# Optimization experiments

Measured on AMD Instinct MI355X. Metric: run time of the kernel, lower is better.

Reference implementation:

```python
import jax, jax.numpy as jnp
import numpy as np

EPS = 1e-5
N_NODES = 50000


def batchnorm(x, gamma, beta):
    # training-mode BatchNorm1d: batch mean, biased variance
    mean = jnp.mean(x, axis=0)
    var = jnp.mean(jnp.square(x - mean), axis=0)
    return (x - mean) * jax.lax.rsqrt(var + EPS) * gamma + beta


def setup_inputs() -> dict:
    key = jax.random.key(0)
    ks = jax.random.split(key, 8)
    N, E, D_IN, D_H, D_OUT = N_NODES, 800000, 128, 128, 128
    feat = jax.random.normal(ks[0], (N, D_IN), dtype=jnp.float32)
    w = jax.random.uniform(ks[1], (E,), dtype=jnp.float32)
    # xavier_uniform with relu gain for Q and W
    gain = float(np.sqrt(2.0))
    bq = gain * np.sqrt(6.0 / (D_IN + D_H))
    bw = gain * np.sqrt(6.0 / (D_IN + D_H + D_OUT))
    Q_w = jax.random.uniform(ks[2], (D_H, D_IN), minval=-bq, maxval=bq, dtype=jnp.float32)
    W_w = jax.random.uniform(ks[3], (D_OUT, D_IN + D_H), minval=-bw, maxval=bw, dtype=jnp.float32)
    Q_b = jnp.zeros((D_H,), jnp.float32)
    W_b = jnp.zeros((D_OUT,), jnp.float32)
    gamma2 = jnp.ones((D_OUT,), jnp.float32)
    beta2 = jnp.zeros((D_OUT,), jnp.float32)
    src = jax.random.randint(ks[4], (E,), 0, N, dtype=jnp.int32)
    dst = jax.random.randint(ks[5], (E,), 0, N, dtype=jnp.int32)
    return {"feat": feat, "w": w, "Q_w": Q_w, "Q_b": Q_b, "W_w": W_w,
            "W_b": W_b, "gamma2": gamma2, "beta2": beta2, "src": src, "dst": dst}


def reference(feat, w, Q_w, Q_b, W_w, W_b, gamma2, beta2, src, dst):
    N = feat.shape[0]
    # h = dropout(bnorm_two(relu(Q(feat))))  (dropout=0 -> identity; source reuses bnorm_two)
    h = batchnorm(jax.nn.relu(feat @ Q_w.T + Q_b), gamma2, beta2)  # [N, H]
    # weighted neighbor mean: sum_e w_e * h[src_e] scattered to dst, / sum_e w_e
    num = jax.ops.segment_sum(w[:, None] * h[src], dst, num_segments=N)  # [N, H]
    den = jax.ops.segment_sum(w, dst, num_segments=N)  # [N]
    has_msg = den[:, None] != 0
    agg = jnp.where(has_msg, num / jnp.where(has_msg, den[:, None], 1.0), h)
    rst = jnp.concatenate([feat, agg], axis=1) @ W_w.T + W_b  # [N, OUT]
    rst = batchnorm(jax.nn.relu(rst), gamma2, beta2)
    denom = jnp.linalg.norm(rst, axis=1, keepdims=True)
    return rst / jnp.where(denom == 0, 1.0, denom)
```

## Files before the change

kernel.cpp:

```cpp
#include <hip/hip_runtime.h>
#include <stdint.h>


#define BN_EPS 1e-5f
#define NSLOT 32

typedef __attribute__((ext_vector_type(8))) short bf16x8;
typedef __attribute__((ext_vector_type(4))) float f32x4;

static __device__ __forceinline__ unsigned short f2bf(float f) {
    uint32_t u = __builtin_bit_cast(uint32_t, f);
    u += 0x7fffu + ((u >> 16) & 1u);
    return (unsigned short)(u >> 16);
}
static __device__ __forceinline__ float bf_lo(uint32_t u) {
    return __builtin_bit_cast(float, u << 16);
}
static __device__ __forceinline__ float bf_hi(uint32_t u) {
    return __builtin_bit_cast(float, u & 0xffff0000u);
}

static __device__ __forceinline__ void cast_blk(
    const float* __restrict__ src, unsigned short* __restrict__ dst,
    int n, int blk)
{
    int i = (blk * 256 + threadIdx.x) * 4;
    if (i + 3 < n) {
        float4 v = *(const float4*)(src + i);
        ushort4 o;
        o.x = f2bf(v.x); o.y = f2bf(v.y); o.z = f2bf(v.z); o.w = f2bf(v.w);
        *(ushort4*)(dst + i) = o;
    } else {
        for (int j = i; j < n; ++j) dst[j] = f2bf(src[j]);
    }
}

__global__ __launch_bounds__(256) void k_pre(
    const float* __restrict__ feat, unsigned short* __restrict__ featb, int nf,
    const int* __restrict__ dst, int* __restrict__ ccnt, int E, int CB, int HB,
    const float* __restrict__ Qw, unsigned short* __restrict__ Qwb,
    const float* __restrict__ Ww, unsigned short* __restrict__ Wwb)
{
    int b = (int)blockIdx.x;
    if (b < CB) { cast_blk(feat, featb, nf, b); return; }
    b -= CB;
    if (b >= HB) {
        b -= HB;
        if (b < 16) cast_blk(Qw, Qwb, 128 * 128, b);
        else        cast_blk(Ww, Wwb, 128 * 256, b - 16);
        return;
    }
    __shared__ int hcnt[128];
    const int tid = threadIdx.x;
    if (tid < 128) hcnt[tid] = 0;
    __syncthreads();
    const int base_e = b * 2048;
#pragma unroll
    for (int j = 0; j < 8; ++j) {
        int e = base_e + j * 256 + tid;
        if (e < E) atomicAdd(&hcnt[dst[e] >> 9], 1);
    }
    __syncthreads();
    if (tid < 128 && hcnt[tid] > 0) atomicAdd(&ccnt[tid], hcnt[tid]);
}

__global__ __launch_bounds__(128) void k_coffs(
    const int* __restrict__ ccnt, int* __restrict__ coffs,
    int* __restrict__ gcur, int* __restrict__ offs, int N, int E)
{
    __shared__ int w0sum;
    const int t = threadIdx.x;
    const int lane = t & 63, wv = t >> 6;
    int v = ccnt[t];
    int incl = v;
#pragma unroll
    for (int o = 1; o < 64; o <<= 1) {
        int u = __shfl_up(incl, o, 64);
        if (lane >= o) incl += u;
    }
    if (wv == 0 && lane == 63) w0sum = incl;
    __syncthreads();
    int excl = incl - v + (wv ? w0sum : 0);
    coffs[t] = excl;
    gcur[t]  = excl;
    if (t == 127) { coffs[128] = excl + v; offs[N] = E; }
}

template<int K>
static __device__ __forceinline__ void gemm_body(
    int bid,
    const unsigned short* __restrict__ A_lo,
    const unsigned short* __restrict__ A_hi,
    const unsigned short* __restrict__ Bb,
    const float* __restrict__ bias,
    float* __restrict__ Y,
    double* __restrict__ sum, double* __restrict__ sumsq, int N)
{
    constexpr int SA = 72;
    __shared__ unsigned short As[64 * SA];
    __shared__ unsigned short Bs[128 * SA];
    __shared__ float bsum_s[128], bsq_s[128];

    const int tid  = threadIdx.x;
    const int lane = tid & 63;
    const int wv   = tid >> 6;
    const int wr   = wv >> 1;
    const int wc   = wv & 1;
    const int m15  = lane & 15;
    const int quad = lane >> 4;
    const int r0   = bid * 64;

    if (tid < 128) { bsum_s[tid] = 0.f; bsq_s[tid] = 0.f; }

    f32x4 acc[2][4];
#pragma unroll
    for (int rt = 0; rt < 2; ++rt)
#pragma unroll
        for (int ct = 0; ct < 4; ++ct)
            acc[rt][ct] = (f32x4){0.f, 0.f, 0.f, 0.f};

    for (int kc = 0; kc < K; kc += 64) {
        const unsigned short* Ap = (kc < 128) ? A_lo : A_hi;
        const int koff = kc & 127;
#pragma unroll
        for (int i = 0; i < 2; ++i) {
            int idx = i * 256 + tid;
            int row = idx >> 3, seg = idx & 7;
            int gr  = r0 + row; if (gr >= N) gr = N - 1;
            uint4 v = *(const uint4*)(Ap + (size_t)gr * 128 + koff + seg * 8);
            *(uint4*)(As + row * SA + seg * 8) = v;
        }
#pragma unroll
        for (int i = 0; i < 4; ++i) {
            int idx = i * 256 + tid;
            int row = idx >> 3, seg = idx & 7;
            uint4 v = *(const uint4*)(Bb + (size_t)row * K + kc + seg * 8);
            *(uint4*)(Bs + row * SA + seg * 8) = v;
        }
        __syncthreads();

#pragma unroll
        for (int ks = 0; ks < 64; ks += 32) {
            bf16x8 af[2], bfr[4];
#pragma unroll
            for (int rt = 0; rt < 2; ++rt)
                af[rt] = *(const bf16x8*)(As + (wr * 32 + rt * 16 + m15) * SA + ks + quad * 8);
#pragma unroll
            for (int ct = 0; ct < 4; ++ct)
                bfr[ct] = *(const bf16x8*)(Bs + (wc * 64 + ct * 16 + m15) * SA + ks + quad * 8);
#pragma unroll
            for (int rt = 0; rt < 2; ++rt)
#pragma unroll
                for (int ct = 0; ct < 4; ++ct)
                    acc[rt][ct] = __builtin_amdgcn_mfma_f32_16x16x32_bf16(
                        af[rt], bfr[ct], acc[rt][ct], 0, 0, 0);
        }
        __syncthreads();
    }

#pragma unroll
    for (int ct = 0; ct < 4; ++ct) {
        int col = wc * 64 + ct * 16 + m15;
        float bz = bias[col];
        float s = 0.f, q = 0.f;
#pragma unroll
        for (int rt = 0; rt < 2; ++rt) {
#pragma unroll
            for (int reg = 0; reg < 4; ++reg) {
                int row = r0 + wr * 32 + rt * 16 + quad * 4 + reg;
                float vv = fmaxf(acc[rt][ct][reg] + bz, 0.f);
                if (row < N) {
                    Y[(size_t)row * 128 + col] = vv;
                } else {
                    vv = 0.f;
                }
                s += vv; q = fmaf(vv, vv, q);
            }
        }
        s += __shfl_xor(s, 16, 64); s += __shfl_xor(s, 32, 64);
        q += __shfl_xor(q, 16, 64); q += __shfl_xor(q, 32, 64);
        if (quad == 0) {
            atomicAdd(&bsum_s[col], s);
            atomicAdd(&bsq_s[col], q);
        }
    }
    __syncthreads();
    if (tid < 128) {
        const int slot = (bid & (NSLOT - 1)) * 128;
        atomicAdd(&sum[slot + tid],   (double)bsum_s[tid]);
        atomicAdd(&sumsq[slot + tid], (double)bsq_s[tid]);
    }
}

__global__ __launch_bounds__(128) void bn_coef(
    const double* __restrict__ sum, const double* __restrict__ sumsq,
    const float* __restrict__ gamma, const float* __restrict__ beta,
    float* __restrict__ a, float* __restrict__ b, double invN)
{
    const int t = threadIdx.x;
    double ms = 0.0, qs = 0.0;
#pragma unroll
    for (int s = 0; s < NSLOT; ++s) {
        ms += sum[s * 128 + t];
        qs += sumsq[s * 128 + t];
    }
    float mean = (float)(ms * invN);
    float var  = (float)(qs * invN) - mean * mean;
    float sc = rsqrtf(var + BN_EPS) * gamma[t];
    a[t] = sc;
    b[t] = fmaf(-mean, sc, beta[t]);
}

static __device__ __forceinline__ void bin_body(
    int bid,
    const int* __restrict__ src, const int* __restrict__ dst,
    const float* __restrict__ w, int* __restrict__ gcur,
    int4* __restrict__ tmp, int E)
{
    __shared__ int hcnt[128];
    __shared__ int hbase[128];
    const int tid = threadIdx.x;
    if (tid < 128) hcnt[tid] = 0;
    __syncthreads();

    int d8[8], s8[8], slot8[8];
    float w8[8];
#pragma unroll
    for (int j = 0; j < 8; ++j) {
        int e = bid * 2048 + j * 256 + tid;
        if (e < E) {
            d8[j] = dst[e]; s8[j] = src[e]; w8[j] = w[e];
            slot8[j] = atomicAdd(&hcnt[d8[j] >> 9], 1);
        } else d8[j] = -1;
    }
    __syncthreads();
    if (tid < 128 && hcnt[tid] > 0)
        hbase[tid] = atomicAdd(&gcur[tid], hcnt[tid]);
    __syncthreads();
#pragma unroll
    for (int j = 0; j < 8; ++j) {
        if (d8[j] >= 0) {
            int pos = hbase[d8[j] >> 9] + slot8[j];
            tmp[pos] = make_int4(s8[j], __float_as_int(w8[j]), d8[j], 0);
        }
    }
}

__global__ __launch_bounds__(256) void k_bin_gemm(
    const int* __restrict__ src, const int* __restrict__ dst,
    const float* __restrict__ w, int* __restrict__ gcur,
    int4* __restrict__ tmp, int E, int HB,
    const unsigned short* __restrict__ featb,
    const unsigned short* __restrict__ Qwb, const float* __restrict__ Qb,
    float* __restrict__ y1,
    double* __restrict__ sum, double* __restrict__ sumsq, int N)
{
    if ((int)blockIdx.x < HB)
        bin_body(blockIdx.x, src, dst, w, gcur, tmp, E);
    else
        gemm_body<128>(blockIdx.x - HB, featb, featb, Qwb, Qb, y1, sum, sumsq, N);
}

static __device__ __forceinline__ void refine_body(
    int b,
    const int4* __restrict__ tmp, const int* __restrict__ coffs,
    int* __restrict__ offs, int2* __restrict__ epack, int N)
{
    __shared__ int hist[512];
    __shared__ int wpre[4];
    const int d0   = b << 9;
    const int dlim = min(512, N - d0);
    const int tid  = threadIdx.x;
    const int lane = tid & 63, wv = tid >> 6;
    const int start = coffs[b];
    const int end   = coffs[b + 1];

    hist[tid] = 0; hist[tid + 256] = 0;
    __syncthreads();

    for (int p = start + tid; p < end; p += 256)
        atomicAdd(&hist[tmp[p].z - d0], 1);
    __syncthreads();

    int v0 = hist[2 * tid], v1 = hist[2 * tid + 1];
    int s = v0 + v1;
    int incl = s;
#pragma unroll
    for (int o = 1; o < 64; o <<= 1) {
        int t = __shfl_up(incl, o, 64);
        if (lane >= o) incl += t;
    }
    if (lane == 63) wpre[wv] = incl;
    __syncthreads();
    if (tid == 0) {
        int r = 0;
#pragma unroll
        for (int i = 0; i < 4; ++i) { int t = wpre[i]; wpre[i] = r; r += t; }
    }
    __syncthreads();
    int e0 = start + wpre[wv] + incl - s;
    if (2 * tid < dlim)     offs[d0 + 2 * tid]     = e0;
    if (2 * tid + 1 < dlim) offs[d0 + 2 * tid + 1] = e0 + v0;
    hist[2 * tid]     = e0;
    hist[2 * tid + 1] = e0 + v0;
    __syncthreads();

    for (int p = start + tid; p < end; p += 256) {
        int4 rec = tmp[p];
        int pos = atomicAdd(&hist[rec.z - d0], 1);
        epack[pos] = make_int2(rec.x, rec.y);
    }
}

__global__ __launch_bounds__(256) void k_refine_apply(
    const int4* __restrict__ tmp, const int* __restrict__ coffs,
    int* __restrict__ offs, int2* __restrict__ epack, int N, int NB,
    const float* __restrict__ y,
    const float* __restrict__ a, const float* __restrict__ b,
    unsigned short* __restrict__ h, int n)
{
    if ((int)blockIdx.x < NB) {
        refine_body(blockIdx.x, tmp, coffs, offs, epack, N);
    } else {
        int i = ((blockIdx.x - NB) * 256 + threadIdx.x) * 4;
        if (i >= n) return;
        int c = i & 127;
        float4 v  = *(const float4*)(y + i);
        float4 av = *(const float4*)(a + c);
        float4 bv = *(const float4*)(b + c);
        ushort4 o;
        o.x = f2bf(fmaf(av.x, v.x, bv.x));
        o.y = f2bf(fmaf(av.y, v.y, bv.y));
        o.z = f2bf(fmaf(av.z, v.z, bv.z));
        o.w = f2bf(fmaf(av.w, v.w, bv.w));
        *(ushort4*)(h + i) = o;
    }
}

__global__ __launch_bounds__(256) void gather_agg(
    const unsigned short* __restrict__ h,
    const int* __restrict__ offs, const int2* __restrict__ epack,
    unsigned short* __restrict__ aggb, int N)
{
    const int r    = (int)((blockIdx.x * 256u + threadIdx.x) >> 6);
    const int lane = threadIdx.x & 63;
    if (r >= N) return;
    int p = offs[r];
    const int end = offs[r + 1];
    float nx = 0.f, ny = 0.f, den = 0.f;
    for (; p + 3 < end; p += 4) {
        int2 e0 = epack[p],     e1 = epack[p + 1];
        int2 e2 = epack[p + 2], e3 = epack[p + 3];
        uint32_t u0 = *(const uint32_t*)(h + (size_t)e0.x * 128 + 2 * lane);
        uint32_t u1 = *(const uint32_t*)(h + (size_t)e1.x * 128 + 2 * lane);
        uint32_t u2 = *(const uint32_t*)(h + (size_t)e2.x * 128 + 2 * lane);
        uint32_t u3 = *(const uint32_t*)(h + (size_t)e3.x * 128 + 2 * lane);
        float w0 = __int_as_float(e0.y), w1 = __int_as_float(e1.y);
        float w2 = __int_as_float(e2.y), w3 = __int_as_float(e3.y);
        nx = fmaf(w0, bf_lo(u0), nx); ny = fmaf(w0, bf_hi(u0), ny);
        nx = fmaf(w1, bf_lo(u1), nx); ny = fmaf(w1, bf_hi(u1), ny);
        nx = fmaf(w2, bf_lo(u2), nx); ny = fmaf(w2, bf_hi(u2), ny);
        nx = fmaf(w3, bf_lo(u3), nx); ny = fmaf(w3, bf_hi(u3), ny);
        den += (w0 + w1) + (w2 + w3);
    }
    for (; p < end; ++p) {
        int2 e0 = epack[p];
        float w0 = __int_as_float(e0.y);
        uint32_t u0 = *(const uint32_t*)(h + (size_t)e0.x * 128 + 2 * lane);
        nx = fmaf(w0, bf_lo(u0), nx); ny = fmaf(w0, bf_hi(u0), ny);
        den += w0;
    }
    float2 outv;
    if (den != 0.f) {
        float inv = 1.f / den;
        outv.x = nx * inv; outv.y = ny * inv;
    } else {
        uint32_t u = *(const uint32_t*)(h + (size_t)r * 128 + 2 * lane);
        outv.x = bf_lo(u); outv.y = bf_hi(u);
    }
    ushort2 ao; ao.x = f2bf(outv.x); ao.y = f2bf(outv.y);
    *(ushort2*)&aggb[(size_t)r * 128 + 2 * lane] = ao;
}

__global__ __launch_bounds__(256) void gemm_bn2(
    const unsigned short* __restrict__ A_lo,
    const unsigned short* __restrict__ A_hi,
    const unsigned short* __restrict__ Bb,
    const float* __restrict__ bias,
    float* __restrict__ Y,
    double* __restrict__ sum, double* __restrict__ sumsq, int N)
{
    gemm_body<256>(blockIdx.x, A_lo, A_hi, Bb, bias, Y, sum, sumsq, N);
}

__global__ __launch_bounds__(256) void finalize(
    const float* __restrict__ Y2,
    const float* __restrict__ a, const float* __restrict__ b,
    float* __restrict__ out, int N)
{
    __shared__ float sa[128], sb[128];
    const int t = threadIdx.x;
    if (t < 128) { sa[t] = a[t]; sb[t] = b[t]; }
    __syncthreads();
    const int row  = (int)((blockIdx.x * 256u + t) >> 6);
    const int lane = t & 63;
    if (row >= N) return;
    const size_t base = (size_t)row * 128;
    float v0 = fmaf(sa[lane],      Y2[base + lane],      sb[lane]);
    float v1 = fmaf(sa[lane + 64], Y2[base + lane + 64], sb[lane + 64]);
    float ss = fmaf(v0, v0, v1 * v1);
#pragma unroll
    for (int o = 32; o; o >>= 1) ss += __shfl_xor(ss, o, 64);
    float nrm = sqrtf(ss);
    float inv = (nrm == 0.f) ? 1.f : 1.f / nrm;
    out[base + lane]      = v0 * inv;
    out[base + lane + 64] = v1 * inv;
}

extern "C" void kernel_launch(void* const* d_in, const int* in_sizes, int n_in,
                              void* d_out, int out_size, void* d_ws, size_t ws_size,
                              hipStream_t stream)
{
    const float* feat   = (const float*)d_in[0];
    const float* w      = (const float*)d_in[1];
    const float* Q_w    = (const float*)d_in[2];
    const float* Q_b    = (const float*)d_in[3];
    const float* W_w    = (const float*)d_in[4];
    const float* W_b    = (const float*)d_in[5];
    const float* gamma2 = (const float*)d_in[6];
    const float* beta2  = (const float*)d_in[7];
    const int*   src    = (const int*)d_in[8];
    const int*   dst    = (const int*)d_in[9];

    const int N = in_sizes[0] / 128;
    const int E = in_sizes[1];

    float*          y1    = (float*)d_ws;
    unsigned short* featb = (unsigned short*)(y1 + (size_t)N * 128);
    unsigned short* aggb  = featb + (size_t)N * 128;
    unsigned short* h_bf  = aggb + (size_t)N * 128;
    int4*  tmp    = (int4*)(h_bf + (size_t)N * 128);
    int2*  epack  = (int2*)(tmp + E);
    int*   offs   = (int*)(epack + E);
    int*   coffs  = offs + (N + 1);
    int*   gcur   = coffs + 129;
    float* coefs  = (float*)(gcur + 128);
    float* a1 = coefs, *b1 = coefs + 128, *a2 = coefs + 256, *b2 = coefs + 384;
    uintptr_t qp = ((uintptr_t)(coefs + 512) + 15) & ~(uintptr_t)15;
    unsigned short* Qwb = (unsigned short*)qp;
    unsigned short* Wwb = Qwb + 128 * 128;
    uintptr_t sp = ((uintptr_t)(Wwb + 128 * 256) + 15) & ~(uintptr_t)15;
    double* stats = (double*)sp;
    double* sum1   = stats;
    double* sumsq1 = stats + NSLOT * 128;
    double* sum2   = stats + 2 * NSLOT * 128;
    double* sumsq2 = stats + 3 * NSLOT * 128;
    int*   ccnt   = (int*)(stats + 4 * NSLOT * 128);

    hipMemsetAsync(stats, 0,
                   4 * NSLOT * 128 * sizeof(double) + 128 * sizeof(int),
                   stream);

    const double invN = 1.0 / (double)N;
    const int GB = (N + 63) / 64;
    const int NB = (N + 511) >> 9;
    const int CB = (N * 128 / 4 + 255) / 256;
    const int HB = (E + 2047) / 2048;
    const int AB = (N * 128 / 4 + 255) / 256;
    const int QB = 16;
    const int WB = 32;

    k_pre<<<CB + HB + QB + WB, 256, 0, stream>>>(
        feat, featb, N * 128, dst, ccnt, E, CB, HB,
        Q_w, Qwb, W_w, Wwb);
    k_coffs<<<1, 128, 0, stream>>>(ccnt, coffs, gcur, offs, N, E);

    k_bin_gemm<<<HB + GB, 256, 0, stream>>>(
        src, dst, w, gcur, tmp, E, HB,
        featb, Qwb, Q_b, y1, sum1, sumsq1, N);
    bn_coef<<<1, 128, 0, stream>>>(sum1, sumsq1, gamma2, beta2, a1, b1, invN);

    k_refine_apply<<<NB + AB, 256, 0, stream>>>(
        tmp, coffs, offs, epack, N, NB,
        y1, a1, b1, h_bf, N * 128);

    gather_agg<<<(N * 64 + 255) / 256, 256, 0, stream>>>(h_bf, offs, epack, aggb, N);

    gemm_bn2<<<GB, 256, 0, stream>>>(
        featb, aggb, Wwb, W_b, y1 , sum2, sumsq2, N);
    bn_coef<<<1, 128, 0, stream>>>(sum2, sumsq2, gamma2, beta2, a2, b2, invN);
    finalize<<<(N * 64 + 255) / 256, 256, 0, stream>>>(
        y1, a2, b2, (float*)d_out, N);
}
```

Before: 234.4 us.

## Fold first BatchNorm apply into neighbor gather and store pre-BN activations as bf16

The first GEMM now writes relu output directly as bf16 instead of fp32, and the separate elementwise BN-apply pass that produced h is removed. Because BN is affine and the weights are normalized by their sum, the gather aggregates raw activations and applies the BN scale and shift afterwards. The bn_coef launch is merged into the refine kernel as an extra block. The gather is also restructured so each half-wave handles alternate edges with 8-byte loads, reduced by a cross-half shuffle. This cuts one full-size read and write pass plus a launch, at the cost of bf16 rounding before normalization rather than after.

Measured after the change: 227.7 us. 1.03x faster.

```diff
diff --git a/kernel.cpp b/kernel.cpp
--- a/kernel.cpp
+++ b/kernel.cpp
@@ -86,14 +86,14 @@
     if (t == 127) { coffs[128] = excl + v; offs[N] = E; }
 }
 
-template<int K>
+template<int K, bool OUT_BF16>
 static __device__ __forceinline__ void gemm_body(
     int bid,
     const unsigned short* __restrict__ A_lo,
     const unsigned short* __restrict__ A_hi,
     const unsigned short* __restrict__ Bb,
     const float* __restrict__ bias,
-    float* __restrict__ Y,
+    void* __restrict__ Yv,
     double* __restrict__ sum, double* __restrict__ sumsq, int N)
 {
     constexpr int SA = 72;
@@ -170,7 +170,10 @@
                 int row = r0 + wr * 32 + rt * 16 + quad * 4 + reg;
                 float vv = fmaxf(acc[rt][ct][reg] + bz, 0.f);
                 if (row < N) {
-                    Y[(size_t)row * 128 + col] = vv;
+                    if constexpr (OUT_BF16)
+                        ((unsigned short*)Yv)[(size_t)row * 128 + col] = f2bf(vv);
+                    else
+                        ((float*)Yv)[(size_t)row * 128 + col] = vv;
                 } else {
                     vv = 0.f;
                 }
@@ -192,12 +195,11 @@
     }
 }
 
-__global__ __launch_bounds__(128) void bn_coef(
-    const double* __restrict__ sum, const double* __restrict__ sumsq,
+static __device__ __forceinline__ void bn_coef_body(
+    int t, const double* __restrict__ sum, const double* __restrict__ sumsq,
     const float* __restrict__ gamma, const float* __restrict__ beta,
     float* __restrict__ a, float* __restrict__ b, double invN)
 {
-    const int t = threadIdx.x;
     double ms = 0.0, qs = 0.0;
 #pragma unroll
     for (int s = 0; s < NSLOT; ++s) {
@@ -209,6 +211,14 @@
     float sc = rsqrtf(var + BN_EPS) * gamma[t];
     a[t] = sc;
     b[t] = fmaf(-mean, sc, beta[t]);
+}
+
+__global__ __launch_bounds__(128) void bn_coef(
+    const double* __restrict__ sum, const double* __restrict__ sumsq,
+    const float* __restrict__ gamma, const float* __restrict__ beta,
+    float* __restrict__ a, float* __restrict__ b, double invN)
+{
+    bn_coef_body(threadIdx.x, sum, sumsq, gamma, beta, a, b, invN);
 }
 
 static __device__ __forceinline__ void bin_body(
@@ -252,13 +262,14 @@
     int4* __restrict__ tmp, int E, int HB,
     const unsigned short* __restrict__ featb,
     const unsigned short* __restrict__ Qwb, const float* __restrict__ Qb,
-    float* __restrict__ y1,
+    unsigned short* __restrict__ y1b,
     double* __restrict__ sum, double* __restrict__ sumsq, int N)
 {
     if ((int)blockIdx.x < HB)
         bin_body(blockIdx.x, src, dst, w, gcur, tmp, E);
     else
-        gemm_body<128>(blockIdx.x - HB, featb, featb, Qwb, Qb, y1, sum, sumsq, N);
+        gemm_body<128, true>(blockIdx.x - HB, featb, featb, Qwb, Qb, y1b,
+                             sum, sumsq, N);
 }
 
 static __device__ __forceinline__ void refine_body(
@@ -312,74 +323,86 @@
     }
 }
 
-__global__ __launch_bounds__(256) void k_refine_apply(
+__global__ __launch_bounds__(256) void k_bnref(
+    const double* __restrict__ sum, const double* __restrict__ sumsq,
+    const float* __restrict__ gamma, const float* __restrict__ beta,
+    float* __restrict__ a, float* __restrict__ b, double invN,
     const int4* __restrict__ tmp, const int* __restrict__ coffs,
-    int* __restrict__ offs, int2* __restrict__ epack, int N, int NB,
-    const float* __restrict__ y,
+    int* __restrict__ offs, int2* __restrict__ epack, int N)
+{
+    if (blockIdx.x == 0) {
+        if (threadIdx.x < 128)
+            bn_coef_body(threadIdx.x, sum, sumsq, gamma, beta, a, b, invN);
+        return;
+    }
+    refine_body((int)blockIdx.x - 1, tmp, coffs, offs, epack, N);
+}
+
+__global__ __launch_bounds__(256) void gather_agg(
+    const unsigned short* __restrict__ y1b,
+    const int* __restrict__ offs, const int2* __restrict__ epack,
     const float* __restrict__ a, const float* __restrict__ b,
-    unsigned short* __restrict__ h, int n)
-{
-    if ((int)blockIdx.x < NB) {
-        refine_body(blockIdx.x, tmp, coffs, offs, epack, N);
-    } else {
-        int i = ((blockIdx.x - NB) * 256 + threadIdx.x) * 4;
-        if (i >= n) return;
-        int c = i & 127;
-        float4 v  = *(const float4*)(y + i);
-        float4 av = *(const float4*)(a + c);
-        float4 bv = *(const float4*)(b + c);
-        ushort4 o;
-        o.x = f2bf(fmaf(av.x, v.x, bv.x));
-        o.y = f2bf(fmaf(av.y, v.y, bv.y));
-        o.z = f2bf(fmaf(av.z, v.z, bv.z));
-        o.w = f2bf(fmaf(av.w, v.w, bv.w));
-        *(ushort4*)(h + i) = o;
-    }
-}
-
-__global__ __launch_bounds__(256) void gather_agg(
-    const unsigned short* __restrict__ h,
-    const int* __restrict__ offs, const int2* __restrict__ epack,
     unsigned short* __restrict__ aggb, int N)
 {
     const int r    = (int)((blockIdx.x * 256u + threadIdx.x) >> 6);
     const int lane = threadIdx.x & 63;
+    const int li   = lane & 31;
+    const int hf   = lane >> 5;
     if (r >= N) return;
     int p = offs[r];
     const int end = offs[r + 1];
-    float nx = 0.f, ny = 0.f, den = 0.f;
+    float ac0 = 0.f, ac1 = 0.f, ac2 = 0.f, ac3 = 0.f, den = 0.f;
     for (; p + 3 < end; p += 4) {
-        int2 e0 = epack[p],     e1 = epack[p + 1];
-        int2 e2 = epack[p + 2], e3 = epack[p + 3];
-        uint32_t u0 = *(const uint32_t*)(h + (size_t)e0.x * 128 + 2 * lane);
-        uint32_t u1 = *(const uint32_t*)(h + (size_t)e1.x * 128 + 2 * lane);
-        uint32_t u2 = *(const uint32_t*)(h + (size_t)e2.x * 128 + 2 * lane);
-        uint32_t u3 = *(const uint32_t*)(h + (size_t)e3.x * 128 + 2 * lane);
-        float w0 = __int_as_float(e0.y), w1 = __int_as_float(e1.y);
-        float w2 = __int_as_float(e2.y), w3 = __int_as_float(e3.y);
-        nx = fmaf(w0, bf_lo(u0), nx); ny = fmaf(w0, bf_hi(u0), ny);
-        nx = fmaf(w1, bf_lo(u1), nx); ny = fmaf(w1, bf_hi(u1), ny);
-        nx = fmaf(w2, bf_lo(u2), nx); ny = fmaf(w2, bf_hi(u2), ny);
-        nx = fmaf(w3, bf_lo(u3), nx); ny = fmaf(w3, bf_hi(u3), ny);
-        den += (w0 + w1) + (w2 + w3);
-    }
-    for (; p < end; ++p) {
-        int2 e0 = epack[p];
-        float w0 = __int_as_float(e0.y);
-        uint32_t u0 = *(const uint32_t*)(h + (size_t)e0.x * 128 + 2 * lane);
-        nx = fmaf(w0, bf_lo(u0), nx); ny = fmaf(w0, bf_hi(u0), ny);
-        den += w0;
-    }
-    float2 outv;
+        int2 ea = epack[p + hf];
+        int2 eb = epack[p + 2 + hf];
+        uint2 ua = *(const uint2*)(y1b + (size_t)ea.x * 128 + 4 * li);
+        uint2 ub = *(const uint2*)(y1b + (size_t)eb.x * 128 + 4 * li);
+        float wa = __int_as_float(ea.y), wb = __int_as_float(eb.y);
+        ac0 = fmaf(wa, bf_lo(ua.x), ac0); ac1 = fmaf(wa, bf_hi(ua.x), ac1);
+        ac2 = fmaf(wa, bf_lo(ua.y), ac2); ac3 = fmaf(wa, bf_hi(ua.y), ac3);
+        ac0 = fmaf(wb, bf_lo(ub.x), ac0); ac1 = fmaf(wb, bf_hi(ub.x), ac1);
+        ac2 = fmaf(wb, bf_lo(ub.y), ac2); ac3 = fmaf(wb, bf_hi(ub.y), ac3);
+        den += wa + wb;
+    }
+    for (; p + 1 < end; p += 2) {
+        int2 ea = epack[p + hf];
+        uint2 ua = *(const uint2*)(y1b + (size_t)ea.x * 128 + 4 * li);
+        float wa = __int_as_float(ea.y);
+        ac0 = fmaf(wa, bf_lo(ua.x), ac0); ac1 = fmaf(wa, bf_hi(ua.x), ac1);
+        ac2 = fmaf(wa, bf_lo(ua.y), ac2); ac3 = fmaf(wa, bf_hi(ua.y), ac3);
+        den += wa;
+    }
+    if (p < end && hf == 0) {
+        int2 ea = epack[p];
+        uint2 ua = *(const uint2*)(y1b + (size_t)ea.x * 128 + 4 * li);
+        float wa = __int_as_float(ea.y);
+        ac0 = fmaf(wa, bf_lo(ua.x), ac0); ac1 = fmaf(wa, bf_hi(ua.x), ac1);
+        ac2 = fmaf(wa, bf_lo(ua.y), ac2); ac3 = fmaf(wa, bf_hi(ua.y), ac3);
+        den += wa;
+    }
+    ac0 += __shfl_xor(ac0, 32, 64);
+    ac1 += __shfl_xor(ac1, 32, 64);
+    ac2 += __shfl_xor(ac2, 32, 64);
+    ac3 += __shfl_xor(ac3, 32, 64);
+    den += __shfl_xor(den, 32, 64);
+    if (hf) return;
+    const int c = 4 * li;
+    float4 av = *(const float4*)(a + c);
+    float4 bv = *(const float4*)(b + c);
+    float m0, m1, m2, m3;
     if (den != 0.f) {
         float inv = 1.f / den;
-        outv.x = nx * inv; outv.y = ny * inv;
+        m0 = ac0 * inv; m1 = ac1 * inv; m2 = ac2 * inv; m3 = ac3 * inv;
     } else {
-        uint32_t u = *(const uint32_t*)(h + (size_t)r * 128 + 2 * lane);
-        outv.x = bf_lo(u); outv.y = bf_hi(u);
-    }
-    ushort2 ao; ao.x = f2bf(outv.x); ao.y = f2bf(outv.y);
-    *(ushort2*)&aggb[(size_t)r * 128 + 2 * lane] = ao;
+        uint2 u = *(const uint2*)(y1b + (size_t)r * 128 + c);
+        m0 = bf_lo(u.x); m1 = bf_hi(u.x); m2 = bf_lo(u.y); m3 = bf_hi(u.y);
+    }
+    ushort4 o;
+    o.x = f2bf(fmaf(av.x, m0, bv.x));
+    o.y = f2bf(fmaf(av.y, m1, bv.y));
+    o.z = f2bf(fmaf(av.z, m2, bv.z));
+    o.w = f2bf(fmaf(av.w, m3, bv.w));
+    *(ushort4*)(aggb + (size_t)r * 128 + c) = o;
 }
 
 __global__ __launch_bounds__(256) void gemm_bn2(
@@ -390,7 +413,7 @@
     float* __restrict__ Y,
     double* __restrict__ sum, double* __restrict__ sumsq, int N)
 {
-    gemm_body<256>(blockIdx.x, A_lo, A_hi, Bb, bias, Y, sum, sumsq, N);
+    gemm_body<256, false>(blockIdx.x, A_lo, A_hi, Bb, bias, Y, sum, sumsq, N);
 }
 
 __global__ __launch_bounds__(256) void finalize(
@@ -435,11 +458,11 @@
     const int N = in_sizes[0] / 128;
     const int E = in_sizes[1];
 
-    float*          y1    = (float*)d_ws;
-    unsigned short* featb = (unsigned short*)(y1 + (size_t)N * 128);
+    float*          y2    = (float*)d_ws;
+    unsigned short* featb = (unsigned short*)(y2 + (size_t)N * 128);
     unsigned short* aggb  = featb + (size_t)N * 128;
-    unsigned short* h_bf  = aggb + (size_t)N * 128;
-    int4*  tmp    = (int4*)(h_bf + (size_t)N * 128);
+    unsigned short* y1b   = aggb + (size_t)N * 128;
+    int4*  tmp    = (int4*)(y1b + (size_t)N * 128);
     int2*  epack  = (int2*)(tmp + E);
     int*   offs   = (int*)(epack + E);
     int*   coffs  = offs + (N + 1);
@@ -466,7 +489,6 @@
     const int NB = (N + 511) >> 9;
     const int CB = (N * 128 / 4 + 255) / 256;
     const int HB = (E + 2047) / 2048;
-    const int AB = (N * 128 / 4 + 255) / 256;
     const int QB = 16;
     const int WB = 32;
 
@@ -477,18 +499,18 @@
 
     k_bin_gemm<<<HB + GB, 256, 0, stream>>>(
         src, dst, w, gcur, tmp, E, HB,
-        featb, Qwb, Q_b, y1, sum1, sumsq1, N);
-    bn_coef<<<1, 128, 0, stream>>>(sum1, sumsq1, gamma2, beta2, a1, b1, invN);
-
-    k_refine_apply<<<NB + AB, 256, 0, stream>>>(
-        tmp, coffs, offs, epack, N, NB,
-        y1, a1, b1, h_bf, N * 128);
-
-    gather_agg<<<(N * 64 + 255) / 256, 256, 0, stream>>>(h_bf, offs, epack, aggb, N);
+        featb, Qwb, Q_b, y1b, sum1, sumsq1, N);
+
+    k_bnref<<<NB + 1, 256, 0, stream>>>(
+        sum1, sumsq1, gamma2, beta2, a1, b1, invN,
+        tmp, coffs, offs, epack, N);
+
+    gather_agg<<<(N * 64 + 255) / 256, 256, 0, stream>>>(
+        y1b, offs, epack, a1, b1, aggb, N);
 
     gemm_bn2<<<GB, 256, 0, stream>>>(
-        featb, aggb, Wwb, W_b, y1 , sum2, sumsq2, N);
+        featb, aggb, Wwb, W_b, y2, sum2, sumsq2, N);
     bn_coef<<<1, 128, 0, stream>>>(sum2, sumsq2, gamma2, beta2, a2, b2, invN);
     finalize<<<(N * 64 + 255) / 256, 256, 0, stream>>>(
-        y1, a2, b2, (float*)d_out, N);
-}
+        y2, a2, b2, (float*)d_out, N);
+}
```
